# Kernel tuning notes

Measured on AMD Instinct MI355X. Metric: run time of the kernel, lower is better.

The kernel has to match this reference:

```python
import jax, jax.numpy as jnp
import numpy as np

NB = 8            # num_blocks
BS = 96           # block_size = hidden_size // num_blocks
HSF = 1           # hidden_size_factor
LAM = 0.01        # sparsity_threshold (softshrink lambda)
FRAC = 1.0        # hard_thresholding_fraction
SCALE = 0.02


def setup_inputs() -> dict:
    key = jax.random.key(0)
    ks = jax.random.split(key, 9)
    B, C, H, W, D = 2, NB * BS, 32, 32, 32
    x = jax.random.normal(ks[0], (B, C, H, W, D), jnp.float32)
    # complex params stored as separate real/imag float arrays (torch.rand on cfloat
    # fills real and imag independently with U[0,1))
    w1r = SCALE * jax.random.uniform(ks[1], (NB, BS, BS * HSF), jnp.float32)
    w1i = SCALE * jax.random.uniform(ks[2], (NB, BS, BS * HSF), jnp.float32)
    w2r = SCALE * jax.random.uniform(ks[3], (NB, BS, BS * HSF), jnp.float32)
    w2i = SCALE * jax.random.uniform(ks[4], (NB, BS, BS * HSF), jnp.float32)
    b1r = SCALE * jax.random.uniform(ks[5], (NB, BS * HSF), jnp.float32)
    b1i = SCALE * jax.random.uniform(ks[6], (NB, BS * HSF), jnp.float32)
    b2r = SCALE * jax.random.uniform(ks[7], (NB, BS), jnp.float32)
    b2i = SCALE * jax.random.uniform(ks[8], (NB, BS), jnp.float32)
    return {"x": x, "w1r": w1r, "w1i": w1i, "w2r": w2r, "w2i": w2i,
            "b1r": b1r, "b1i": b1i, "b2r": b2r, "b2i": b2i}


def _softshrink(v, lam):
    return jnp.sign(v) * jnp.maximum(jnp.abs(v) - lam, 0.0)


def _gelu_c(z):
    # torch GELU applied to view_as_real => separately on real and imag parts
    return jax.nn.gelu(jnp.real(z), approximate=False) + 1j * jax.nn.gelu(jnp.imag(z), approximate=False)


def reference(x, w1r, w1i, w2r, w2i, b1r, b1i, b2r, b2i):
    bias = x
    B, C, H, W, D = x.shape
    w1 = w1r + 1j * w1i
    w2 = w2r + 1j * w2i
    b1 = b1r + 1j * b1i
    b2 = b2r + 1j * b2i

    xf = jnp.fft.rfftn(x.astype(jnp.float32), axes=(-3, -2, -1), norm='ortho')
    Dr = xf.shape[-1]                      # D//2 + 1
    xf = xf.reshape(B, NB, BS, H, W, Dr)

    total_modes = H * W * D // 2 + 1
    kept = min(int(total_modes * FRAC), Dr)  # original slices only the last freq axis
    xk = xf[..., :kept]                      # (B, nb, bs, H, W, kept)

    # block-diagonal complex GEMM 1 + bias, then GELU on real/imag parts
    h1 = jnp.einsum('bnihwd,nio->bnohwd', xk, w1) + b1[None, :, :, None, None, None]
    h1 = _gelu_c(h1)
    # block-diagonal complex GEMM 2 + bias
    h2 = jnp.einsum('bnihwd,nio->bnohwd', h1, w2) + b2[None, :, :, None, None, None]

    # scatter back into full spectrum (zeros beyond kept modes)
    if kept < Dr:
        h2 = jnp.pad(h2, ((0, 0), (0, 0), (0, 0), (0, 0), (0, 0), (0, Dr - kept)))

    # softshrink on real/imag parts
    z = _softshrink(jnp.real(h2), LAM) + 1j * _softshrink(jnp.imag(h2), LAM)
    z = z.reshape(B, C, H, W, Dr)
    out = jnp.fft.irfftn(z, s=(H, W, D), axes=(-3, -2, -1), norm='ortho')
    return out.astype(x.dtype) + bias
```

## Files before the change

### kernel.cpp

```cpp
#include <hip/hip_runtime.h>
#include <math.h>


#define CH    768
#define DR    17
#define PLANE 544
#define NVOL  49152
#define CSTRIDE 17408
#define ORTHO 0.0055242717280199026f
#define TWOPI_32 0.19634954084936207f

typedef __bf16 bf16x8 __attribute__((ext_vector_type(8)));
typedef float  f32x4  __attribute__((ext_vector_type(4)));

#define MFMA __builtin_amdgcn_mfma_f32_16x16x32_bf16

__device__ __forceinline__ float gelu_f(float v) {
    return 0.5f * v * (1.0f + erff(v * 0.7071067811865475f));
}
__device__ __forceinline__ float sshrink(float v) {
    float a = fabsf(v) - 0.01f;
    return a > 0.f ? copysignf(a, v) : 0.f;
}
__device__ __forceinline__ bf16x8 ld8(const __bf16* p) { return *(const bf16x8*)p; }
__device__ __forceinline__ void split2(float v, __bf16* h, __bf16* l) {
    __bf16 hh = (__bf16)v;
    *h = hh;
    *l = (__bf16)(v - (float)hh);
}

__device__ __align__(16) __bf16 gEf[4][1024];
__device__ __align__(16) __bf16 gEb[4][1024];
__device__ __align__(16) __bf16 gC [4][1024];

__global__ void k0_tables() {
    int idx = blockIdx.x * 256 + threadIdx.x;
    if (idx >= 1024) return;
    int c = idx & 31;
    int r = idx >> 5;
    float ang = TWOPI_32 * (float)((r * c) & 31);
    float s, co; sincosf(ang, &s, &co);
    __bf16 h, l;
    split2(co, &h, &l);  gEf[0][idx] = h; gEf[1][idx] = l;
                         gEb[0][idx] = h; gEb[1][idx] = l;
    split2(-s, &h, &l);  gEf[2][idx] = h; gEf[3][idx] = l;
    split2(s, &h, &l);   gEb[2][idx] = h; gEb[3][idx] = l;
    float cf = (c == 0 || c == 16) ? 1.f : (c < DR ? 2.f : 0.f);
    split2(cf * co, &h, &l); gC[0][idx] = h; gC[1][idx] = l;
    split2(-cf * s, &h, &l); gC[2][idx] = h; gC[3][idx] = l;
}

__global__ __launch_bounds__(256) void k1_fwd_dw(const float* __restrict__ x,
                                                 float2* __restrict__ A) {
    __shared__ __align__(16) __bf16 sArh[32][40], sArl[32][40], sAih[32][40], sAil[32][40];
    const int t = threadIdx.x;
    const int wave = t >> 6, lane = t & 63, row = lane & 15, quad = lane >> 4;
    const int m0 = (wave >> 1) * 16, n0 = (wave & 1) * 16;
    const size_t pb = (size_t)blockIdx.x * 1024;

    const float* xp = x + pb + (size_t)(m0 + row) * 32 + quad * 8;
    f32x4 x0 = *(const f32x4*)xp;
    f32x4 x1 = *(const f32x4*)(xp + 4);
    bf16x8 xh, xl;
    #pragma unroll
    for (int j = 0; j < 4; j++) { __bf16 h = (__bf16)x0[j]; xh[j] = h; xl[j] = (__bf16)(x0[j] - (float)h); }
    #pragma unroll
    for (int j = 0; j < 4; j++) { __bf16 h = (__bf16)x1[j]; xh[4+j] = h; xl[4+j] = (__bf16)(x1[j] - (float)h); }

    {
        const int ed = (n0 + row) * 32 + quad * 8;
        bf16x8 erh = *(const bf16x8*)&gEf[0][ed];
        bf16x8 erl = *(const bf16x8*)&gEf[1][ed];
        bf16x8 eih = *(const bf16x8*)&gEf[2][ed];
        bf16x8 eil = *(const bf16x8*)&gEf[3][ed];
        f32x4 ar = {0.f,0.f,0.f,0.f}, ai = {0.f,0.f,0.f,0.f};
        ar = MFMA(xh, erh, ar, 0,0,0); ar = MFMA(xh, erl, ar, 0,0,0); ar = MFMA(xl, erh, ar, 0,0,0);
        ai = MFMA(xh, eih, ai, 0,0,0); ai = MFMA(xh, eil, ai, 0,0,0); ai = MFMA(xl, eih, ai, 0,0,0);
        #pragma unroll
        for (int r4 = 0; r4 < 4; r4++) {
            int w = m0 + quad * 4 + r4, kd = n0 + row;
            split2(ar[r4], &sArh[kd][w], &sArl[kd][w]);
            split2(ai[r4], &sAih[kd][w], &sAil[kd][w]);
        }
    }
    __syncthreads();
    {
        const int ew = (m0 + row) * 32 + quad * 8;
        bf16x8 frh = *(const bf16x8*)&gEf[0][ew];
        bf16x8 frl = *(const bf16x8*)&gEf[1][ew];
        bf16x8 fih = *(const bf16x8*)&gEf[2][ew];
        bf16x8 fil = *(const bf16x8*)&gEf[3][ew];
        bf16x8 arh = ld8(&sArh[n0 + row][quad * 8]);
        bf16x8 arl = ld8(&sArl[n0 + row][quad * 8]);
        bf16x8 aih = ld8(&sAih[n0 + row][quad * 8]);
        bf16x8 ail = ld8(&sAil[n0 + row][quad * 8]);
        f32x4 rp = {0.f,0.f,0.f,0.f}, rm = {0.f,0.f,0.f,0.f}, im = {0.f,0.f,0.f,0.f};
        rp = MFMA(frh, arh, rp, 0,0,0); rp = MFMA(frh, arl, rp, 0,0,0); rp = MFMA(frl, arh, rp, 0,0,0);
        rm = MFMA(fih, aih, rm, 0,0,0); rm = MFMA(fih, ail, rm, 0,0,0); rm = MFMA(fil, aih, rm, 0,0,0);
        im = MFMA(frh, aih, im, 0,0,0); im = MFMA(frh, ail, im, 0,0,0); im = MFMA(frl, aih, im, 0,0,0);
        im = MFMA(fih, arh, im, 0,0,0); im = MFMA(fih, arl, im, 0,0,0); im = MFMA(fil, arh, im, 0,0,0);
        const size_t ab = (size_t)blockIdx.x * PLANE;
        int kd = n0 + row;
        if (kd < DR) {
            #pragma unroll
            for (int r4 = 0; r4 < 4; r4++) {
                int kw = m0 + quad * 4 + r4;
                A[ab + kw * DR + kd] = make_float2((rp[r4] - rm[r4]) * ORTHO, im[r4] * ORTHO);
            }
        }
    }
}

template <bool INV>
__global__ __launch_bounds__(256) void k2_fft_h(float2* __restrict__ A) {
    __shared__ float2 twf[32];
    __shared__ __align__(16) __bf16 sEr[32][40],  sEi[32][40];
    __shared__ __align__(16) __bf16 sBr[272][40], sBi[272][40];
    const int t = threadIdx.x;
    if (t < 32) {
        float s, c; sincosf(-TWOPI_32 * (float)t, &s, &c);
        twf[t] = make_float2(c, INV ? -s : s);
    }
    __syncthreads();
    for (int idx = t; idx < 1024; idx += 256) {
        int kh = idx >> 5, h = idx & 31;
        float2 e = twf[(kh * h) & 31];
        sEr[kh][h] = (__bf16)e.x;
        sEi[kh][h] = (__bf16)e.y;
    }
    const int p0g = blockIdx.x * 272;
    const size_t cb = (size_t)blockIdx.y * CSTRIDE;
    for (int idx = t; idx < 8704; idx += 256) {
        int h = idx / 272, p = idx - h * 272;
        float2 v = A[cb + (size_t)h * PLANE + p0g + p];
        sBr[p][h] = (__bf16)v.x;
        sBi[p][h] = (__bf16)v.y;
    }
    __syncthreads();
    const int wave = t >> 6, lane = t & 63, row = lane & 15, quad = lane >> 4;
    for (int j = wave; j < 34; j += 4) {
        int mt = j & 1, nt = j >> 1;
        int m0 = mt * 16, n0 = nt * 16;
        bf16x8 ar = ld8(&sEr[m0 + row][quad * 8]);
        bf16x8 ai = ld8(&sEi[m0 + row][quad * 8]);
        bf16x8 br = ld8(&sBr[n0 + row][quad * 8]);
        bf16x8 bi = ld8(&sBi[n0 + row][quad * 8]);
        f32x4 rp = {0.f,0.f,0.f,0.f}, rm = {0.f,0.f,0.f,0.f}, im = {0.f,0.f,0.f,0.f};
        rp = MFMA(ar, br, rp, 0, 0, 0);
        rm = MFMA(ai, bi, rm, 0, 0, 0);
        im = MFMA(ar, bi, im, 0, 0, 0);
        im = MFMA(ai, br, im, 0, 0, 0);
        int p = p0g + n0 + row;
        #pragma unroll
        for (int r = 0; r < 4; r++) {
            int kh = m0 + quad * 4 + r;
            A[cb + (size_t)kh * PLANE + p] = make_float2(rp[r] - rm[r], im[r]);
        }
    }
}

__global__ __launch_bounds__(256) void k3_mix(float2* __restrict__ A,
    const float* __restrict__ w1r, const float* __restrict__ w1i,
    const float* __restrict__ w2r, const float* __restrict__ w2i,
    const float* __restrict__ b1r, const float* __restrict__ b1i,
    const float* __restrict__ b2r, const float* __restrict__ b2i) {
    __shared__ __align__(16) __bf16 sWr[96][104], sWi[96][104];
    __shared__ __align__(16) __bf16 sXr[64][104], sXi[64][104];
    const int t = threadIdx.x;
    const int chunk = blockIdx.x, bn = blockIdx.y;
    const int b = bn >> 3, n = bn & 7;
    const size_t base = (size_t)(b * CH + n * 96) * CSTRIDE + chunk * 64;

    const float* W1r = w1r + n * 9216;
    const float* W1i = w1i + n * 9216;
    for (int idx = t; idx < 9216; idx += 256) {
        int i = idx / 96, o = idx - i * 96;
        sWr[o][i] = (__bf16)W1r[idx];
        sWi[o][i] = (__bf16)W1i[idx];
    }
    for (int idx = t; idx < 6144; idx += 256) {
        int i = idx >> 6, p = idx & 63;
        float2 v = A[base + (size_t)i * CSTRIDE + p];
        sXr[p][i] = (__bf16)v.x;
        sXi[p][i] = (__bf16)v.y;
    }
    __syncthreads();

    const int wave = t >> 6, lane = t & 63, row = lane & 15, quad = lane >> 4;
    float h1s[6][8];

    #pragma unroll
    for (int q = 0; q < 6; q++) {
        int job = wave * 6 + q, mt = job >> 2, nt = job & 3;
        int m0 = mt * 16, p0 = nt * 16;
        f32x4 rp = {0.f,0.f,0.f,0.f}, rm = {0.f,0.f,0.f,0.f}, im = {0.f,0.f,0.f,0.f};
        #pragma unroll
        for (int ks = 0; ks < 3; ks++) {
            int k0 = ks * 32 + quad * 8;
            bf16x8 ar = ld8(&sWr[m0 + row][k0]);
            bf16x8 ai = ld8(&sWi[m0 + row][k0]);
            bf16x8 br = ld8(&sXr[p0 + row][k0]);
            bf16x8 bi = ld8(&sXi[p0 + row][k0]);
            rp = MFMA(ar, br, rp, 0, 0, 0);
            rm = MFMA(ai, bi, rm, 0, 0, 0);
            im = MFMA(ar, bi, im, 0, 0, 0);
            im = MFMA(ai, br, im, 0, 0, 0);
        }
        #pragma unroll
        for (int r = 0; r < 4; r++) {
            int o = m0 + quad * 4 + r;
            float hr = b1r[n * 96 + o] + rp[r] - rm[r];
            float hi = b1i[n * 96 + o] + im[r];
            h1s[q][r]     = gelu_f(hr);
            h1s[q][4 + r] = gelu_f(hi);
        }
    }
    __syncthreads();

    #pragma unroll
    for (int q = 0; q < 6; q++) {
        int job = wave * 6 + q, mt = job >> 2, nt = job & 3;
        int m0 = mt * 16, p0 = nt * 16;
        int p = p0 + row;
        #pragma unroll
        for (int r = 0; r < 4; r++) {
            int o = m0 + quad * 4 + r;
            sXr[p][o] = (__bf16)h1s[q][r];
            sXi[p][o] = (__bf16)h1s[q][4 + r];
        }
    }
    const float* W2r = w2r + n * 9216;
    const float* W2i = w2i + n * 9216;
    for (int idx = t; idx < 9216; idx += 256) {
        int i = idx / 96, o = idx - i * 96;
        sWr[o][i] = (__bf16)W2r[idx];
        sWi[o][i] = (__bf16)W2i[idx];
    }
    __syncthreads();

    #pragma unroll
    for (int q = 0; q < 6; q++) {
        int job = wave * 6 + q, mt = job >> 2, nt = job & 3;
        int m0 = mt * 16, p0 = nt * 16;
        f32x4 rp = {0.f,0.f,0.f,0.f}, rm = {0.f,0.f,0.f,0.f}, im = {0.f,0.f,0.f,0.f};
        #pragma unroll
        for (int ks = 0; ks < 3; ks++) {
            int k0 = ks * 32 + quad * 8;
            bf16x8 ar = ld8(&sWr[m0 + row][k0]);
            bf16x8 ai = ld8(&sWi[m0 + row][k0]);
            bf16x8 br = ld8(&sXr[p0 + row][k0]);
            bf16x8 bi = ld8(&sXi[p0 + row][k0]);
            rp = MFMA(ar, br, rp, 0, 0, 0);
            rm = MFMA(ai, bi, rm, 0, 0, 0);
            im = MFMA(ar, bi, im, 0, 0, 0);
            im = MFMA(ai, br, im, 0, 0, 0);
        }
        int p = p0 + row;
        #pragma unroll
        for (int r = 0; r < 4; r++) {
            int o = m0 + quad * 4 + r;
            float hr = sshrink(b2r[n * 96 + o] + rp[r] - rm[r]);
            float hi = sshrink(b2i[n * 96 + o] + im[r]);
            A[base + (size_t)o * CSTRIDE + p] = make_float2(hr, hi);
        }
    }
}

__global__ __launch_bounds__(256) void k5_inv_wd(const float2* __restrict__ A,
                                                 const float* __restrict__ x,
                                                 float* __restrict__ out) {
    __shared__ __align__(16) __bf16 sZrh[32][40], sZrl[32][40], sZih[32][40], sZil[32][40];
    const int t = threadIdx.x;
    const int wave = t >> 6, lane = t & 63, row = lane & 15, quad = lane >> 4;
    const int m0 = (wave >> 1) * 16, n0 = (wave & 1) * 16;
    const size_t ab = (size_t)blockIdx.x * PLANE;
    const size_t pb = (size_t)blockIdx.x * 1024;
    const int d = n0 + row;

    float xres[4];
    #pragma unroll
    for (int r4 = 0; r4 < 4; r4++)
        xres[r4] = x[pb + (size_t)(m0 + quad * 4 + r4) * 32 + d];

    for (int idx = t; idx < PLANE; idx += 256) {
        int kw = idx / DR, kd = idx - kw * DR;
        float2 v = A[ab + idx];
        split2(v.x, &sZrh[kd][kw], &sZrl[kd][kw]);
        split2(v.y, &sZih[kd][kw], &sZil[kd][kw]);
    }
    for (int idx = t; idx < 480; idx += 256) {
        int kd = DR + (idx >> 5), kw = idx & 31;
        sZrh[kd][kw] = (__bf16)0.f; sZrl[kd][kw] = (__bf16)0.f;
        sZih[kd][kw] = (__bf16)0.f; sZil[kd][kw] = (__bf16)0.f;
    }
    __syncthreads();

    const int e1 = (m0 + row) * 32 + quad * 8;
    bf16x8 erh = *(const bf16x8*)&gEb[0][e1];
    bf16x8 erl = *(const bf16x8*)&gEb[1][e1];
    bf16x8 eih = *(const bf16x8*)&gEb[2][e1];
    bf16x8 eil = *(const bf16x8*)&gEb[3][e1];
    bf16x8 zrh = ld8(&sZrh[n0 + row][quad * 8]);
    bf16x8 zrl = ld8(&sZrl[n0 + row][quad * 8]);
    bf16x8 zih = ld8(&sZih[n0 + row][quad * 8]);
    bf16x8 zil = ld8(&sZil[n0 + row][quad * 8]);
    f32x4 rp = {0.f,0.f,0.f,0.f}, rm = {0.f,0.f,0.f,0.f}, im = {0.f,0.f,0.f,0.f};
    rp = MFMA(erh, zrh, rp, 0,0,0); rp = MFMA(erh, zrl, rp, 0,0,0); rp = MFMA(erl, zrh, rp, 0,0,0);
    rm = MFMA(eih, zih, rm, 0,0,0); rm = MFMA(eih, zil, rm, 0,0,0); rm = MFMA(eil, zih, rm, 0,0,0);
    im = MFMA(erh, zih, im, 0,0,0); im = MFMA(erh, zil, im, 0,0,0); im = MFMA(erl, zih, im, 0,0,0);
    im = MFMA(eih, zrh, im, 0,0,0); im = MFMA(eih, zrl, im, 0,0,0); im = MFMA(eil, zrh, im, 0,0,0);
    __syncthreads();
    #pragma unroll
    for (int r4 = 0; r4 < 4; r4++) {
        int w = m0 + quad * 4 + r4, kd = n0 + row;
        split2(rp[r4] - rm[r4], &sZrh[w][kd], &sZrl[w][kd]);
        split2(im[r4],          &sZih[w][kd], &sZil[w][kd]);
    }
    __syncthreads();

    const int c2 = d * 32 + quad * 8;
    bf16x8 crh = *(const bf16x8*)&gC[0][c2];
    bf16x8 crl = *(const bf16x8*)&gC[1][c2];
    bf16x8 cih = *(const bf16x8*)&gC[2][c2];
    bf16x8 cil = *(const bf16x8*)&gC[3][c2];
    bf16x8 grh = ld8(&sZrh[m0 + row][quad * 8]);
    bf16x8 grl = ld8(&sZrl[m0 + row][quad * 8]);
    bf16x8 gih = ld8(&sZih[m0 + row][quad * 8]);
    bf16x8 gil = ld8(&sZil[m0 + row][quad * 8]);
    f32x4 acc = {0.f,0.f,0.f,0.f};
    acc = MFMA(grh, crh, acc, 0,0,0); acc = MFMA(grh, crl, acc, 0,0,0); acc = MFMA(grl, crh, acc, 0,0,0);
    acc = MFMA(gih, cih, acc, 0,0,0); acc = MFMA(gih, cil, acc, 0,0,0); acc = MFMA(gil, cih, acc, 0,0,0);
    #pragma unroll
    for (int r4 = 0; r4 < 4; r4++) {
        int w = m0 + quad * 4 + r4;
        out[pb + (size_t)w * 32 + d] = acc[r4] * ORTHO + xres[r4];
    }
}

extern "C" void kernel_launch(void* const* d_in, const int* in_sizes, int n_in,
                              void* d_out, int out_size, void* d_ws, size_t ws_size,
                              hipStream_t stream) {
    const float* x   = (const float*)d_in[0];
    const float* w1r = (const float*)d_in[1];
    const float* w1i = (const float*)d_in[2];
    const float* w2r = (const float*)d_in[3];
    const float* w2i = (const float*)d_in[4];
    const float* b1r = (const float*)d_in[5];
    const float* b1i = (const float*)d_in[6];
    const float* b2r = (const float*)d_in[7];
    const float* b2i = (const float*)d_in[8];
    float* out = (float*)d_out;
    float2* A = (float2*)d_ws;

    k0_tables<<<4, 256, 0, stream>>>();
    k1_fwd_dw<<<NVOL, 256, 0, stream>>>(x, A);
    k2_fft_h<false><<<dim3(2, 1536), 256, 0, stream>>>(A);
    k3_mix<<<dim3(272, 16), 256, 0, stream>>>(A, w1r, w1i, w2r, w2i, b1r, b1i, b2r, b2i);
    k2_fft_h<true><<<dim3(2, 1536), 256, 0, stream>>>(A);
    k5_inv_wd<<<NVOL, 256, 0, stream>>>(A, x, out);
}
```

Baseline: 893.2 us.

## Pre-transpose weights to bf16 globally and read twiddles from global tables

A new prologue kernel converts and transposes the complex mixing weights to bf16 once per call into global buffers. The mix kernel then loads weight fragments straight from global memory (L2-cached) instead of rebuilding them in shared memory in every block. The H-axis FFT kernel drops its per-block twiddle computation and shared-memory staging and loads register fragments from the precomputed global tables. This cuts redundant per-block conversion work and shared-memory use, which may raise occupancy, but it adds global-load latency inside the MFMA loops.

Measured after the change: 873.3 us. -2.2%, faster.

```diff
diff --git a/kernel.cpp b/kernel.cpp
--- a/kernel.cpp
+++ b/kernel.cpp
@@ -48,6 +48,21 @@
     float cf = (c == 0 || c == 16) ? 1.f : (c < DR ? 2.f : 0.f);
     split2(cf * co, &h, &l); gC[0][idx] = h; gC[1][idx] = l;
     split2(-cf * s, &h, &l); gC[2][idx] = h; gC[3][idx] = l;
+}
+
+__device__ __align__(16) __bf16 gW1r[73728], gW1i[73728], gW2r[73728], gW2i[73728];
+
+__global__ void k0w(const float* __restrict__ w1r, const float* __restrict__ w1i,
+                    const float* __restrict__ w2r, const float* __restrict__ w2i) {
+    int idx = blockIdx.x * 256 + threadIdx.x;
+    if (idx >= 73728) return;
+    int i = idx % 96, no = idx / 96;
+    int o = no % 96, n = no / 96;
+    int src = n * 9216 + i * 96 + o;
+    gW1r[idx] = (__bf16)w1r[src];
+    gW1i[idx] = (__bf16)w1i[src];
+    gW2r[idx] = (__bf16)w2r[src];
+    gW2i[idx] = (__bf16)w2i[src];
 }
 
 __global__ __launch_bounds__(256) void k1_fwd_dw(const float* __restrict__ x,
@@ -113,21 +128,8 @@
 
 template <bool INV>
 __global__ __launch_bounds__(256) void k2_fft_h(float2* __restrict__ A) {
-    __shared__ float2 twf[32];
-    __shared__ __align__(16) __bf16 sEr[32][40],  sEi[32][40];
     __shared__ __align__(16) __bf16 sBr[272][40], sBi[272][40];
     const int t = threadIdx.x;
-    if (t < 32) {
-        float s, c; sincosf(-TWOPI_32 * (float)t, &s, &c);
-        twf[t] = make_float2(c, INV ? -s : s);
-    }
-    __syncthreads();
-    for (int idx = t; idx < 1024; idx += 256) {
-        int kh = idx >> 5, h = idx & 31;
-        float2 e = twf[(kh * h) & 31];
-        sEr[kh][h] = (__bf16)e.x;
-        sEi[kh][h] = (__bf16)e.y;
-    }
     const int p0g = blockIdx.x * 272;
     const size_t cb = (size_t)blockIdx.y * CSTRIDE;
     for (int idx = t; idx < 8704; idx += 256) {
@@ -138,11 +140,17 @@
     }
     __syncthreads();
     const int wave = t >> 6, lane = t & 63, row = lane & 15, quad = lane >> 4;
+    const __bf16* Er = gEf[0];
+    const __bf16* Ei = INV ? gEb[2] : gEf[2];
+    bf16x8 er0 = *(const bf16x8*)&Er[row * 32 + quad * 8];
+    bf16x8 ei0 = *(const bf16x8*)&Ei[row * 32 + quad * 8];
+    bf16x8 er1 = *(const bf16x8*)&Er[(16 + row) * 32 + quad * 8];
+    bf16x8 ei1 = *(const bf16x8*)&Ei[(16 + row) * 32 + quad * 8];
     for (int j = wave; j < 34; j += 4) {
         int mt = j & 1, nt = j >> 1;
         int m0 = mt * 16, n0 = nt * 16;
-        bf16x8 ar = ld8(&sEr[m0 + row][quad * 8]);
-        bf16x8 ai = ld8(&sEi[m0 + row][quad * 8]);
+        bf16x8 ar = mt ? er1 : er0;
+        bf16x8 ai = mt ? ei1 : ei0;
         bf16x8 br = ld8(&sBr[n0 + row][quad * 8]);
         bf16x8 bi = ld8(&sBi[n0 + row][quad * 8]);
         f32x4 rp = {0.f,0.f,0.f,0.f}, rm = {0.f,0.f,0.f,0.f}, im = {0.f,0.f,0.f,0.f};
@@ -160,24 +168,14 @@
 }
 
 __global__ __launch_bounds__(256) void k3_mix(float2* __restrict__ A,
-    const float* __restrict__ w1r, const float* __restrict__ w1i,
-    const float* __restrict__ w2r, const float* __restrict__ w2i,
     const float* __restrict__ b1r, const float* __restrict__ b1i,
     const float* __restrict__ b2r, const float* __restrict__ b2i) {
-    __shared__ __align__(16) __bf16 sWr[96][104], sWi[96][104];
     __shared__ __align__(16) __bf16 sXr[64][104], sXi[64][104];
     const int t = threadIdx.x;
     const int chunk = blockIdx.x, bn = blockIdx.y;
     const int b = bn >> 3, n = bn & 7;
     const size_t base = (size_t)(b * CH + n * 96) * CSTRIDE + chunk * 64;
 
-    const float* W1r = w1r + n * 9216;
-    const float* W1i = w1i + n * 9216;
-    for (int idx = t; idx < 9216; idx += 256) {
-        int i = idx / 96, o = idx - i * 96;
-        sWr[o][i] = (__bf16)W1r[idx];
-        sWi[o][i] = (__bf16)W1i[idx];
-    }
     for (int idx = t; idx < 6144; idx += 256) {
         int i = idx >> 6, p = idx & 63;
         float2 v = A[base + (size_t)i * CSTRIDE + p];
@@ -187,6 +185,10 @@
     __syncthreads();
 
     const int wave = t >> 6, lane = t & 63, row = lane & 15, quad = lane >> 4;
+    const __bf16* W1r = &gW1r[n * 9216];
+    const __bf16* W1i = &gW1i[n * 9216];
+    const __bf16* W2r = &gW2r[n * 9216];
+    const __bf16* W2i = &gW2i[n * 9216];
     float h1s[6][8];
 
     #pragma unroll
@@ -197,8 +199,8 @@
         #pragma unroll
         for (int ks = 0; ks < 3; ks++) {
             int k0 = ks * 32 + quad * 8;
-            bf16x8 ar = ld8(&sWr[m0 + row][k0]);
-            bf16x8 ai = ld8(&sWi[m0 + row][k0]);
+            bf16x8 ar = ld8(&W1r[(m0 + row) * 96 + k0]);
+            bf16x8 ai = ld8(&W1i[(m0 + row) * 96 + k0]);
             bf16x8 br = ld8(&sXr[p0 + row][k0]);
             bf16x8 bi = ld8(&sXi[p0 + row][k0]);
             rp = MFMA(ar, br, rp, 0, 0, 0);
@@ -229,13 +231,6 @@
             sXi[p][o] = (__bf16)h1s[q][4 + r];
         }
     }
-    const float* W2r = w2r + n * 9216;
-    const float* W2i = w2i + n * 9216;
-    for (int idx = t; idx < 9216; idx += 256) {
-        int i = idx / 96, o = idx - i * 96;
-        sWr[o][i] = (__bf16)W2r[idx];
-        sWi[o][i] = (__bf16)W2i[idx];
-    }
     __syncthreads();
 
     #pragma unroll
@@ -246,8 +241,8 @@
         #pragma unroll
         for (int ks = 0; ks < 3; ks++) {
             int k0 = ks * 32 + quad * 8;
-            bf16x8 ar = ld8(&sWr[m0 + row][k0]);
-            bf16x8 ai = ld8(&sWi[m0 + row][k0]);
+            bf16x8 ar = ld8(&W2r[(m0 + row) * 96 + k0]);
+            bf16x8 ai = ld8(&W2i[(m0 + row) * 96 + k0]);
             bf16x8 br = ld8(&sXr[p0 + row][k0]);
             bf16x8 bi = ld8(&sXi[p0 + row][k0]);
             rp = MFMA(ar, br, rp, 0, 0, 0);
@@ -353,9 +348,10 @@
     float2* A = (float2*)d_ws;
 
     k0_tables<<<4, 256, 0, stream>>>();
+    k0w<<<288, 256, 0, stream>>>(w1r, w1i, w2r, w2i);
     k1_fwd_dw<<<NVOL, 256, 0, stream>>>(x, A);
     k2_fft_h<false><<<dim3(2, 1536), 256, 0, stream>>>(A);
-    k3_mix<<<dim3(272, 16), 256, 0, stream>>>(A, w1r, w1i, w2r, w2i, b1r, b1i, b2r, b2i);
+    k3_mix<<<dim3(272, 16), 256, 0, stream>>>(A, b1r, b1i, b2r, b2i);
     k2_fft_h<true><<<dim3(2, 1536), 256, 0, stream>>>(A);
     k5_inv_wd<<<NVOL, 256, 0, stream>>>(A, x, out);
 }
```
